# Performance work log

Hardware: AMD Instinct MI355X
Metric: run time of the kernel (lower is better)

## Reference

```python
import jax, jax.numpy as jnp
import numpy as np

POS_THR = 0.7
NEG_THR = 0.3
SAMPLE_BATCH = 256
POS_FRAC = 0.5
B, K, H, W, G = 8, 9, 64, 64, 128
A = K * H * W  # 36864 total anchors


def _make_boxes(key, lead_shape, img=1024.0, wmin=16.0, wmax=256.0):
    k1, k2 = jax.random.split(key)
    ctr = jax.random.uniform(k1, lead_shape + (2,), minval=0.0, maxval=img)
    wh = jax.random.uniform(k2, lead_shape + (2,), minval=wmin, maxval=wmax)
    return jnp.concatenate([ctr - wh / 2, ctr + wh / 2], axis=-1)


def setup_inputs() -> dict:
    key = jax.random.key(0)
    k1, k2, k3, k4 = jax.random.split(key, 4)
    return {
        "cls_logits": jax.random.normal(k1, (B, K, H, W), dtype=jnp.float32),
        "bbox_pred": jax.random.normal(k2, (B, 4 * K, H, W), dtype=jnp.float32) * 0.1,
        "anchors": _make_boxes(k3, (A,)),
        "gt_boxes": _make_boxes(k4, (B, G)),
    }


def _compute_iou(a, g):
    # a: [A,4], g: [G,4] -> [A,G]
    lt = jnp.maximum(a[:, None, :2], g[None, :, :2])
    rb = jnp.minimum(a[:, None, 2:], g[None, :, 2:])
    wh = jnp.clip(rb - lt, 0.0)
    inter = wh[..., 0] * wh[..., 1]
    area_a = (a[:, 2] - a[:, 0]) * (a[:, 3] - a[:, 1])
    area_g = (g[:, 2] - g[:, 0]) * (g[:, 3] - g[:, 1])
    return inter / (area_a[:, None] + area_g[None, :] - inter + 1e-6)


def _encode(anchors, gt):
    aw = anchors[:, 2] - anchors[:, 0]
    ah = anchors[:, 3] - anchors[:, 1]
    acx = (anchors[:, 0] + anchors[:, 2]) / 2
    acy = (anchors[:, 1] + anchors[:, 3]) / 2
    gw = gt[:, 2] - gt[:, 0]
    gh = gt[:, 3] - gt[:, 1]
    gcx = (gt[:, 0] + gt[:, 2]) / 2
    gcy = (gt[:, 1] + gt[:, 3]) / 2
    return jnp.stack([(gcx - acx) / aw, (gcy - acy) / ah,
                      jnp.log(gw / aw), jnp.log(gh / ah)], axis=1)


def _subsample(labels, mask, target, key):
    # deterministic-key analog of torch.randperm subsampling: random priorities,
    # keep the `target` highest-priority anchors of the masked class.
    score = jnp.where(mask, jax.random.uniform(key, labels.shape), -1.0)
    order = jnp.argsort(-score)
    rank = jnp.zeros_like(order).at[order].set(jnp.arange(order.shape[0]))
    keep = mask & (rank < target)
    return jnp.where(mask & ~keep, -1, labels)


def _per_image(cls_i, box_i, anchors, gt, key):
    iou = _compute_iou(anchors, gt)                      # [A,G]
    max_iou = iou.max(axis=1)
    matched_gt_idx = iou.argmax(axis=1)
    labels = jnp.where(max_iou < NEG_THR, 0, -1)
    labels = jnp.where(max_iou >= POS_THR, 1, labels)
    matched_anchor_idx = iou.argmax(axis=0)              # [G]
    labels = labels.at[matched_anchor_idx].set(1)        # force best anchor per gt
    bbox_targets = _encode(anchors, gt[matched_gt_idx])  # [A,4]

    k1, k2 = jax.random.split(key)
    pos_mask0 = labels == 1
    num_pos = pos_mask0.sum()
    target_pos = jnp.minimum(jnp.int32(SAMPLE_BATCH * POS_FRAC), num_pos)
    labels = _subsample(labels, pos_mask0, target_pos, k1)
    neg_mask0 = labels == 0
    num_neg = neg_mask0.sum()
    target_neg = jnp.minimum(SAMPLE_BATCH - target_pos, num_neg)
    labels = _subsample(labels, neg_mask0, target_neg, k2)

    valid = (labels >= 0).astype(cls_i.dtype)
    z = (labels == 1).astype(cls_i.dtype)
    # BCEWithLogits: softplus(x) - x*z
    bce = jax.nn.softplus(cls_i) - cls_i * z
    cls_loss = (bce * valid).sum() / jnp.maximum(valid.sum(), 1.0)

    pos = (labels == 1).astype(cls_i.dtype)
    d = box_i - bbox_targets
    ad = jnp.abs(d)
    sl1 = jnp.where(ad < 1.0, 0.5 * d * d, ad - 0.5)     # SmoothL1, beta=1
    bbox_loss = (sl1 * pos[:, None]).sum() / jnp.maximum(4.0 * pos.sum(), 1.0)
    return cls_loss, bbox_loss


def reference(cls_logits, bbox_pred, anchors, gt_boxes):
    b = cls_logits.shape[0]
    cls = cls_logits.transpose(0, 2, 3, 1).reshape(b, -1)          # [B,A]
    box = bbox_pred.transpose(0, 2, 3, 1).reshape(b, -1, 4)        # [B,A,4]
    keys = jax.random.split(jax.random.key(42), b)
    cls_l, box_l = jax.vmap(_per_image, in_axes=(0, 0, None, 0, 0))(
        cls, box, anchors, gt_boxes, keys)
    cls_loss = cls_l.mean()
    bbox_loss = box_l.mean()
    return jnp.stack([cls_loss, bbox_loss, cls_loss + bbox_loss])
```

## Files before the change

### kernel.cpp

```cpp
#include <hip/hip_runtime.h>
#include <stdint.h>
#include <limits.h>

#define PARTITIONABLE 1

#define B_ 8
#define K_ 9
#define H_ 64
#define W_ 64
#define G_ 128
#define A_ 36864
#define HALF_A 18432
#define QUART_A 9216
#define NBUCK 8192
#define CAP 1024
#define NBEST 4096
#define NLAB  1152

struct KeyParams { uint32_t k[B_][4]; };

__host__ __device__ static inline uint32_t rotl32(uint32_t x, int r) {
  return (x << r) | (x >> (32 - r));
}

__host__ __device__ static inline void tf2x32(uint32_t k0, uint32_t k1,
                                              uint32_t x0, uint32_t x1,
                                              uint32_t& o0, uint32_t& o1) {
  uint32_t ks2 = k0 ^ k1 ^ 0x1BD11BDAu;
  x0 += k0; x1 += k1;
#define TF_R(r) { x0 += x1; x1 = rotl32(x1, r); x1 ^= x0; }
  TF_R(13) TF_R(15) TF_R(26) TF_R(6)
  x0 += k1;  x1 += ks2 + 1u;
  TF_R(17) TF_R(29) TF_R(16) TF_R(24)
  x0 += ks2; x1 += k0 + 2u;
  TF_R(13) TF_R(15) TF_R(26) TF_R(6)
  x0 += k0;  x1 += k1 + 3u;
  TF_R(17) TF_R(29) TF_R(16) TF_R(24)
  x0 += k1;  x1 += ks2 + 4u;
  TF_R(13) TF_R(15) TF_R(26) TF_R(6)
  x0 += ks2; x1 += k0 + 5u;
#undef TF_R
  o0 = x0; o1 = x1;
}

__device__ static inline uint32_t anchor_vbits(uint32_t k0, uint32_t k1, int a) {
  uint32_t o0, o1;
#if PARTITIONABLE
  tf2x32(k0, k1, 0u, (uint32_t)a, o0, o1);
  return (o0 ^ o1) >> 9;
#else
  if (a < HALF_A) { tf2x32(k0, k1, (uint32_t)a, (uint32_t)(a + HALF_A), o0, o1); return o0 >> 9; }
  else            { tf2x32(k0, k1, (uint32_t)(a - HALF_A), (uint32_t)a, o0, o1); return o1 >> 9; }
#endif
}

__device__ static inline float area_of(float x0, float y0, float x1, float y1) {
#pragma clang fp contract(off)
  return (x1 - x0) * (y1 - y0);
}

__device__ static inline float iou_fn(float a0, float a1, float a2, float a3,
                                      float g0, float g1, float g2, float g3) {
#pragma clang fp contract(off)
  float ltx = fmaxf(a0, g0), lty = fmaxf(a1, g1);
  float rbx = fminf(a2, g2), rby = fminf(a3, g3);
  float w = rbx - ltx; w = (w < 0.f) ? 0.f : w;
  float h = rby - lty; h = (h < 0.f) ? 0.f : h;
  float inter  = w * h;
  float area_a = (a2 - a0) * (a3 - a1);
  float area_g = (g2 - g0) * (g3 - g1);
  return inter / (area_a + area_g - inter + 1e-6f);
}

__device__ static inline float iou_pre_a(float a0, float a1, float a2, float a3,
                                         float area_a,
                                         float g0, float g1, float g2, float g3) {
#pragma clang fp contract(off)
  float ltx = fmaxf(a0, g0), lty = fmaxf(a1, g1);
  float rbx = fminf(a2, g2), rby = fminf(a3, g3);
  float w = rbx - ltx; w = (w < 0.f) ? 0.f : w;
  float h = rby - lty; h = (h < 0.f) ? 0.f : h;
  float inter  = w * h;
  float area_g = (g2 - g0) * (g3 - g1);
  return inter / (area_a + area_g - inter + 1e-6f);
}

__device__ static inline void encode4(float4 an, float4 gg, float* tt) {
#pragma clang fp contract(off)
  float aw  = an.z - an.x,            ah  = an.w - an.y;
  float acx = (an.x + an.z) * 0.5f,   acy = (an.y + an.w) * 0.5f;
  float gw  = gg.z - gg.x,            gh  = gg.w - gg.y;
  float gcx = (gg.x + gg.z) * 0.5f,   gcy = (gg.y + gg.w) * 0.5f;
  tt[0] = (gcx - acx) / aw;
  tt[1] = (gcy - acy) / ah;
  tt[2] = logf(gw / aw);
  tt[3] = logf(gh / ah);
}

__device__ static inline int block_reduce_int(int v, int* sh) {
  int t = threadIdx.x;
  sh[t] = v; __syncthreads();
  for (int s = 128; s > 0; s >>= 1) { if (t < s) sh[t] += sh[t + s]; __syncthreads(); }
  int r = sh[0]; __syncthreads();
  return r;
}
__device__ static inline float block_reduce_float(float v, float* sh) {
  int t = threadIdx.x;
  sh[t] = v; __syncthreads();
  for (int s = 128; s > 0; s >>= 1) { if (t < s) sh[t] += sh[t + s]; __syncthreads(); }
  float r = sh[0]; __syncthreads();
  return r;
}

__device__ static inline unsigned long long pack_vi(float v, int a) {
  return ((unsigned long long)__float_as_uint(v) << 32) | (uint32_t)(~(uint32_t)a);
}

__global__ __launch_bounds__(256) void fused_iou_k(const float* __restrict__ anchors,
                                                   const float* __restrict__ gtb,
                                                   int* __restrict__ labels,
                                                   int* __restrict__ mgt,
                                                   uint32_t* __restrict__ vpos,
                                                   uint32_t* __restrict__ vneg,
                                                   int* __restrict__ ghist,
                                                   int* __restrict__ counts,
                                                   unsigned long long* __restrict__ gmax,
                                                   KeyParams kp) {
  __shared__ unsigned long long sp[256];
  __shared__ float4 gts[G_];
  __shared__ int red[256];
  const int bid = blockIdx.x;
  const int t = threadIdx.x;

  if (bid < NBEST) {
    const int bg = bid & 1023;
    const int base = (bid >> 10) * QUART_A;
    float4 gg = ((const float4*)gtb)[bg];
    float v0 = -1.f, v1 = -1.f, v2 = -1.f, v3 = -1.f;
    int   i0 = 0,    i1 = 0,    i2 = 0,    i3 = 0;
    for (int a = base + t; a < base + QUART_A; a += 1024) {
      float4 an0 = ((const float4*)anchors)[a];
      float4 an1 = ((const float4*)anchors)[a + 256];
      float4 an2 = ((const float4*)anchors)[a + 512];
      float4 an3 = ((const float4*)anchors)[a + 768];
      float w0 = iou_fn(an0.x, an0.y, an0.z, an0.w, gg.x, gg.y, gg.z, gg.w);
      float w1 = iou_fn(an1.x, an1.y, an1.z, an1.w, gg.x, gg.y, gg.z, gg.w);
      float w2 = iou_fn(an2.x, an2.y, an2.z, an2.w, gg.x, gg.y, gg.z, gg.w);
      float w3 = iou_fn(an3.x, an3.y, an3.z, an3.w, gg.x, gg.y, gg.z, gg.w);
      if (w0 > v0) { v0 = w0; i0 = a; }
      if (w1 > v1) { v1 = w1; i1 = a + 256; }
      if (w2 > v2) { v2 = w2; i2 = a + 512; }
      if (w3 > v3) { v3 = w3; i3 = a + 768; }
    }
    unsigned long long p = pack_vi(v0, i0);
    unsigned long long q = pack_vi(v1, i1); if (q > p) p = q;
    q = pack_vi(v2, i2); if (q > p) p = q;
    q = pack_vi(v3, i3); if (q > p) p = q;
    sp[t] = p; __syncthreads();
    for (int s = 128; s > 0; s >>= 1) {
      if (t < s) { if (sp[t + s] > sp[t]) sp[t] = sp[t + s]; }
      __syncthreads();
    }
    if (t == 0) atomicMax(&gmax[bg], sp[0]);
    return;
  }

  const int r = bid - NBEST;
  const int b = r / (A_ / 256);
  const int xb = r % (A_ / 256);
  for (int i = t; i < G_; i += 256) gts[i] = ((const float4*)gtb)[b * G_ + i];
  __syncthreads();
  const int a = xb * 256 + t;
  float4 an = ((const float4*)anchors)[a];
  float area_a = area_of(an.x, an.y, an.z, an.w);
  float bv = -1.f; int bi = 0;
#pragma unroll 4
  for (int g = 0; g < G_; g++) {
    float4 gg = gts[g];
    float v = iou_pre_a(an.x, an.y, an.z, an.w, area_a,
                        gg.x, gg.y, gg.z, gg.w);
    if (v > bv) { bv = v; bi = g; }
  }
  int lb = (bv < 0.3f) ? 0 : ((bv >= 0.7f) ? 1 : -1);
  size_t idx = (size_t)b * A_ + a;
  uint32_t vp = anchor_vbits(kp.k[b][0], kp.k[b][1], a);
  uint32_t vn = anchor_vbits(kp.k[b][2], kp.k[b][3], a);
  labels[idx] = lb;
  mgt[idx]    = bi;
  vpos[idx]   = vp;
  vneg[idx]   = vn;
  if (lb == 1)      atomicAdd(&ghist[(b * 2 + 0) * NBUCK + (vp >> 10)], 1);
  else if (lb == 0) atomicAdd(&ghist[(b * 2 + 1) * NBUCK + (vn >> 10)], 1);
  int packed = (lb == 1 ? 1 : 0) | ((lb == 0 ? 1 : 0) << 16);
  int rr = block_reduce_int(packed, red);
  if (t == 0) {
    atomicAdd(&counts[b * 2 + 0], rr & 0xFFFF);
    atomicAdd(&counts[b * 2 + 1], rr >> 16);
  }
}

__global__ void force_k(const unsigned long long* __restrict__ gmax,
                        int* __restrict__ labels,
                        const uint32_t* __restrict__ vpos,
                        const uint32_t* __restrict__ vneg,
                        int* __restrict__ ghist,
                        int* __restrict__ counts) {
  int tg = blockIdx.x * 256 + threadIdx.x;
  int b = tg / G_;
  int a = (int)(~(uint32_t)(gmax[tg] & 0xFFFFFFFFull));
  size_t idx = (size_t)b * A_ + a;
  int old = atomicExch(&labels[idx], 1);
  if (old != 1) {
    atomicAdd(&counts[b * 2 + 0], 1);
    atomicAdd(&ghist[(b * 2 + 0) * NBUCK + (vpos[idx] >> 10)], 1);
    if (old == 0) {
      atomicSub(&counts[b * 2 + 1], 1);
      atomicSub(&ghist[(b * 2 + 1) * NBUCK + (vneg[idx] >> 10)], 1);
    }
  }
}

__global__ __launch_bounds__(256) void cutoff_k(const int* __restrict__ ghist,
                                                const int* __restrict__ counts,
                                                int* __restrict__ cbR,
                                                int* __restrict__ targets) {
  const int row = blockIdx.x;
  const int b = row >> 1, c = row & 1;
  const int t = threadIdx.x;
  __shared__ int seg[256];
  int npos = counts[b * 2 + 0], nneg = counts[b * 2 + 1];
  int tp = npos < 128 ? npos : 128;
  int tn = 256 - tp; if (nneg < tn) tn = nneg;
  const int target = (c == 0) ? tp : tn;
  const int* hist = ghist + (size_t)row * NBUCK;
  { int s = 0; const int base = t * 32;
    for (int i = 0; i < 32; i++) s += hist[base + i];
    seg[t] = s; }
  __syncthreads();
  if (t == 0) {
    int cb = INT_MAX, R = 0;
    if (target > 0) {
      int cum = 0, si = -1;
      for (int i = 255; i >= 0; i--) { if (cum + seg[i] >= target) { si = i; break; } cum += seg[i]; }
      for (int j = si * 32 + 31; j >= si * 32; j--) {
        if (cum + hist[j] >= target) { cb = j; R = target - cum; break; }
        cum += hist[j];
      }
    }
    cbR[row * 2 + 0] = cb;
    cbR[row * 2 + 1] = R;
    targets[row] = target;
  }
}

__global__ __launch_bounds__(256) void cand_k(const int* __restrict__ labels,
                                              const uint32_t* __restrict__ vpos,
                                              const uint32_t* __restrict__ vneg,
                                              const int* __restrict__ cbR,
                                              int* __restrict__ ccnt,
                                              uint32_t* __restrict__ cvv,
                                              int* __restrict__ cii) {
  const int b = blockIdx.y;
  const int a = blockIdx.x * 256 + threadIdx.x;
  size_t idx = (size_t)b * A_ + a;
  int lb = labels[idx];
  if (lb < 0) return;
  int c = (lb == 1) ? 0 : 1;
  int row = b * 2 + c;
  uint32_t v = (c == 0 ? vpos : vneg)[idx];
  if ((int)(v >> 10) == cbR[row * 2]) {
    int p = atomicAdd(&ccnt[row], 1);
    if (p < CAP) { cvv[row * CAP + p] = v; cii[row * CAP + p] = a; }
  }
}

__global__ __launch_bounds__(256) void loss_k(const float* __restrict__ anchors,
                                              const float* __restrict__ gtb,
                                              const float* __restrict__ cls,
                                              const float* __restrict__ boxp,
                                              const int* __restrict__ labels,
                                              const int* __restrict__ mgt,
                                              const uint32_t* __restrict__ vpos,
                                              const uint32_t* __restrict__ vneg,
                                              const int* __restrict__ cbR,
                                              const int* __restrict__ ccnt,
                                              const uint32_t* __restrict__ cvv,
                                              const int* __restrict__ cii,
                                              float* __restrict__ bsums) {
  const int b = blockIdx.y;
  const int a = blockIdx.x * 256 + threadIdx.x;
  const int t = threadIdx.x;
  __shared__ float redf[256];
  float sb = 0.f, ss = 0.f;
  size_t idx = (size_t)b * A_ + a;
  int lb = labels[idx];
  if (lb >= 0) {
    int c = (lb == 1) ? 0 : 1;
    int row = b * 2 + c;
    uint32_t v = (c == 0 ? vpos : vneg)[idx];
    int bucket = (int)(v >> 10);
    int cb = cbR[row * 2];
    bool kept = bucket > cb;
    if (!kept && bucket == cb) {
      int c2 = ccnt[row]; if (c2 > CAP) c2 = CAP;
      int R = cbR[row * 2 + 1];
      int r = 0;
      for (int j = 0; j < c2; j++) {
        uint32_t vj = cvv[row * CAP + j]; int ij = cii[row * CAP + j];
        if (vj > v || (vj == v && ij < a)) r++;
      }
      kept = (r < R);
    }
    if (kept) {
      int kk = a % K_; int hw = a / K_; int hh = hw / W_; int wx = hw % W_;
      float x  = cls[(((size_t)b * K_ + kk) * H_ + hh) * W_ + wx];
      float sp = fmaxf(x, 0.f) + log1pf(expf(-fabsf(x)));
      sb = (lb == 1) ? (sp - x) : sp;
      if (lb == 1) {
        float4 an = ((const float4*)anchors)[a];
        int    mg = mgt[idx];
        float4 gg = ((const float4*)gtb)[b * G_ + mg];
        float tt[4]; encode4(an, gg, tt);
        for (int cc = 0; cc < 4; cc++) {
          float p = boxp[(((size_t)b * (4 * K_) + (4 * kk + cc)) * H_ + hh) * W_ + wx];
          float d = p - tt[cc];
          float ad = fabsf(d);
          ss += (ad < 1.f) ? (0.5f * d * d) : (ad - 0.5f);
        }
      }
    }
  }
  float sbT = block_reduce_float(sb, redf);
  float ssT = block_reduce_float(ss, redf);
  if (t == 0) {
    if (sbT != 0.f) atomicAdd(&bsums[b * 2 + 0], sbT);
    if (ssT != 0.f) atomicAdd(&bsums[b * 2 + 1], ssT);
  }
}

__global__ void final_k(const float* __restrict__ bsums, const int* __restrict__ targets,
                        float* __restrict__ out) {
  if (threadIdx.x == 0 && blockIdx.x == 0) {
    float cl = 0.f, bl = 0.f;
    for (int b = 0; b < B_; b++) {
      int tp = targets[b * 2 + 0], tn = targets[b * 2 + 1];
      cl += bsums[b * 2 + 0] / fmaxf((float)(tp + tn), 1.f);
      bl += bsums[b * 2 + 1] / fmaxf(4.f * (float)tp, 1.f);
    }
    cl *= 0.125f; bl *= 0.125f;
    out[0] = cl; out[1] = bl; out[2] = cl + bl;
  }
}

static void compute_keys(KeyParams& kp) {
  const uint32_t r0 = 0u, r1 = 42u;
#if PARTITIONABLE
  for (int b = 0; b < B_; b++) {
    uint32_t kb0, kb1;
    tf2x32(r0, r1, 0u, (uint32_t)b, kb0, kb1);
    uint32_t a0, a1, c0, c1;
    tf2x32(kb0, kb1, 0u, 0u, a0, a1);
    tf2x32(kb0, kb1, 0u, 1u, c0, c1);
    kp.k[b][0] = a0; kp.k[b][1] = a1; kp.k[b][2] = c0; kp.k[b][3] = c1;
  }
#else
  uint32_t o0[8], o1[8], flat[16];
  for (int i = 0; i < 8; i++) tf2x32(r0, r1, (uint32_t)i, (uint32_t)(8 + i), o0[i], o1[i]);
  for (int i = 0; i < 8; i++) { flat[i] = o0[i]; flat[8 + i] = o1[i]; }
  for (int b = 0; b < B_; b++) {
    uint32_t kb0 = flat[2 * b], kb1 = flat[2 * b + 1];
    uint32_t a0, b0, a1, b1;
    tf2x32(kb0, kb1, 0u, 2u, a0, b0);
    tf2x32(kb0, kb1, 1u, 3u, a1, b1);
    kp.k[b][0] = a0; kp.k[b][1] = a1; kp.k[b][2] = b0; kp.k[b][3] = b1;
  }
#endif
}

extern "C" void kernel_launch(void* const* d_in, const int* in_sizes, int n_in,
                              void* d_out, int out_size, void* d_ws, size_t ws_size,
                              hipStream_t stream) {
  const float* cls     = (const float*)d_in[0];
  const float* boxp    = (const float*)d_in[1];
  const float* anchors = (const float*)d_in[2];
  const float* gtb     = (const float*)d_in[3];
  float* out = (float*)d_out;

  uint8_t* w = (uint8_t*)d_ws;
  unsigned long long* gmax = (unsigned long long*)w;
  int*      ghist   = (int*)(w + 8192);
  int*      counts  = (int*)(w + 532480);
  int*      ccnt    = counts + 16;
  float*    bsums   = (float*)(ccnt + 16);
  int*      labels  = (int*)(w + 532672);
  int*      mgt     = labels + (size_t)B_ * A_;
  uint32_t* vpos    = (uint32_t*)(mgt + (size_t)B_ * A_);
  uint32_t* vneg    = vpos + (size_t)B_ * A_;
  int*      cbR     = (int*)(vneg + (size_t)B_ * A_);
  int*      targets = cbR + 32;
  uint32_t* cvv     = (uint32_t*)(targets + 16);
  int*      cii     = (int*)(cvv + 16 * CAP);

  KeyParams kp;
  compute_keys(kp);

  (void)hipMemsetAsync(w, 0, 532672, stream);
  fused_iou_k<<<NBEST + NLAB, 256, 0, stream>>>(anchors, gtb, labels, mgt,
                                                vpos, vneg, ghist, counts, gmax, kp);
  force_k<<<(B_ * G_) / 256, 256, 0, stream>>>(gmax, labels, vpos, vneg, ghist, counts);
  cutoff_k<<<16, 256, 0, stream>>>(ghist, counts, cbR, targets);
  cand_k<<<dim3(A_ / 256, B_), 256, 0, stream>>>(labels, vpos, vneg, cbR, ccnt, cvv, cii);
  loss_k<<<dim3(A_ / 256, B_), 256, 0, stream>>>(anchors, gtb, cls, boxp, labels, mgt,
                                                 vpos, vneg, cbR, ccnt, cvv, cii, bsums);
  final_k<<<1, 64, 0, stream>>>(bsums, targets, out);
}
```

Baseline: 175.7 us.

## Fuse per-GT best-anchor search into per-anchor IoU pass via LDS atomics

Removes the separate 4096 blocks that recomputed IoU per GT box to find each GT's best anchor. The per-anchor label blocks now also produce it: each thread visits the GT boxes in a staggered order (starting at its own lane modulo 128) and does shared-memory 64-bit atomicMax into duplicated per-GT slots. The slots are then merged and pushed to global gmax. This halves the IoU computation but adds one LDS atomic per IoU, which may contend or serialize. Argmax tie-breaking is preserved through packed value and index encoding.

```diff
diff --git a/kernel.cpp b/kernel.cpp
--- a/kernel.cpp
+++ b/kernel.cpp
@@ -11,10 +11,8 @@
 #define G_ 128
 #define A_ 36864
 #define HALF_A 18432
-#define QUART_A 9216
 #define NBUCK 8192
 #define CAP 1024
-#define NBEST 4096
 #define NLAB  1152
 
 struct KeyParams { uint32_t k[B_][4]; };
@@ -59,19 +57,6 @@
   return (x1 - x0) * (y1 - y0);
 }
 
-__device__ static inline float iou_fn(float a0, float a1, float a2, float a3,
-                                      float g0, float g1, float g2, float g3) {
-#pragma clang fp contract(off)
-  float ltx = fmaxf(a0, g0), lty = fmaxf(a1, g1);
-  float rbx = fminf(a2, g2), rby = fminf(a3, g3);
-  float w = rbx - ltx; w = (w < 0.f) ? 0.f : w;
-  float h = rby - lty; h = (h < 0.f) ? 0.f : h;
-  float inter  = w * h;
-  float area_a = (a2 - a0) * (a3 - a1);
-  float area_g = (g2 - g0) * (g3 - g1);
-  return inter / (area_a + area_g - inter + 1e-6f);
-}
-
 __device__ static inline float iou_pre_a(float a0, float a1, float a2, float a3,
                                          float area_a,
                                          float g0, float g1, float g2, float g3) {
@@ -112,10 +97,6 @@
   return r;
 }
 
-__device__ static inline unsigned long long pack_vi(float v, int a) {
-  return ((unsigned long long)__float_as_uint(v) << 32) | (uint32_t)(~(uint32_t)a);
-}
-
 __global__ __launch_bounds__(256) void fused_iou_k(const float* __restrict__ anchors,
                                                    const float* __restrict__ gtb,
                                                    int* __restrict__ labels,
@@ -126,61 +107,53 @@
                                                    int* __restrict__ counts,
                                                    unsigned long long* __restrict__ gmax,
                                                    KeyParams kp) {
-  __shared__ unsigned long long sp[256];
-  __shared__ float4 gts[G_];
+  __shared__ float2 gp01[2 * G_];
+  __shared__ float2 gp23[2 * G_];
+  __shared__ unsigned long long slot2[2 * G_];
   __shared__ int red[256];
   const int bid = blockIdx.x;
   const int t = threadIdx.x;
-
-  if (bid < NBEST) {
-    const int bg = bid & 1023;
-    const int base = (bid >> 10) * QUART_A;
-    float4 gg = ((const float4*)gtb)[bg];
-    float v0 = -1.f, v1 = -1.f, v2 = -1.f, v3 = -1.f;
-    int   i0 = 0,    i1 = 0,    i2 = 0,    i3 = 0;
-    for (int a = base + t; a < base + QUART_A; a += 1024) {
-      float4 an0 = ((const float4*)anchors)[a];
-      float4 an1 = ((const float4*)anchors)[a + 256];
-      float4 an2 = ((const float4*)anchors)[a + 512];
-      float4 an3 = ((const float4*)anchors)[a + 768];
-      float w0 = iou_fn(an0.x, an0.y, an0.z, an0.w, gg.x, gg.y, gg.z, gg.w);
-      float w1 = iou_fn(an1.x, an1.y, an1.z, an1.w, gg.x, gg.y, gg.z, gg.w);
-      float w2 = iou_fn(an2.x, an2.y, an2.z, an2.w, gg.x, gg.y, gg.z, gg.w);
-      float w3 = iou_fn(an3.x, an3.y, an3.z, an3.w, gg.x, gg.y, gg.z, gg.w);
-      if (w0 > v0) { v0 = w0; i0 = a; }
-      if (w1 > v1) { v1 = w1; i1 = a + 256; }
-      if (w2 > v2) { v2 = w2; i2 = a + 512; }
-      if (w3 > v3) { v3 = w3; i3 = a + 768; }
-    }
-    unsigned long long p = pack_vi(v0, i0);
-    unsigned long long q = pack_vi(v1, i1); if (q > p) p = q;
-    q = pack_vi(v2, i2); if (q > p) p = q;
-    q = pack_vi(v3, i3); if (q > p) p = q;
-    sp[t] = p; __syncthreads();
-    for (int s = 128; s > 0; s >>= 1) {
-      if (t < s) { if (sp[t + s] > sp[t]) sp[t] = sp[t + s]; }
-      __syncthreads();
-    }
-    if (t == 0) atomicMax(&gmax[bg], sp[0]);
-    return;
-  }
-
-  const int r = bid - NBEST;
-  const int b = r / (A_ / 256);
-  const int xb = r % (A_ / 256);
-  for (int i = t; i < G_; i += 256) gts[i] = ((const float4*)gtb)[b * G_ + i];
+  const int b  = bid / (A_ / 256);
+  const int xb = bid % (A_ / 256);
+
+  if (t < G_) {
+    float4 gg = ((const float4*)gtb)[b * G_ + t];
+    float2 p01; p01.x = gg.x; p01.y = gg.y;
+    float2 p23; p23.x = gg.z; p23.y = gg.w;
+    gp01[t] = p01; gp01[t + G_] = p01;
+    gp23[t] = p23; gp23[t + G_] = p23;
+  }
+  slot2[t] = 0ull;
   __syncthreads();
+
   const int a = xb * 256 + t;
   float4 an = ((const float4*)anchors)[a];
   float area_a = area_of(an.x, an.y, an.z, an.w);
-  float bv = -1.f; int bi = 0;
+  const int t7 = t & (G_ - 1);
+  const unsigned long long alow = (unsigned long long)(~(uint32_t)a);
+  unsigned long long blp = 0ull;
 #pragma unroll 4
-  for (int g = 0; g < G_; g++) {
-    float4 gg = gts[g];
+  for (int s = 0; s < G_; s++) {
+    const int gi = t7 + s;
+    float2 p01 = gp01[gi];
+    float2 p23 = gp23[gi];
     float v = iou_pre_a(an.x, an.y, an.z, an.w, area_a,
-                        gg.x, gg.y, gg.z, gg.w);
-    if (v > bv) { bv = v; bi = g; }
-  }
+                        p01.x, p01.y, p23.x, p23.y);
+    unsigned long long hi = (unsigned long long)__float_as_uint(v) << 32;
+    unsigned long long lp = hi | (unsigned)((gi & (G_ - 1)) ^ (G_ - 1));
+    if (lp > blp) blp = lp;
+    atomicMax(&slot2[gi], hi | alow);
+  }
+  __syncthreads();
+  if (t < G_) {
+    unsigned long long p = slot2[t];
+    unsigned long long q = slot2[t + G_];
+    if (q > p) p = q;
+    atomicMax(&gmax[b * G_ + t], p);
+  }
+
+  float bv = __uint_as_float((uint32_t)(blp >> 32));
+  int   bi = ((int)(blp & (unsigned long long)(G_ - 1))) ^ (G_ - 1);
   int lb = (bv < 0.3f) ? 0 : ((bv >= 0.7f) ? 1 : -1);
   size_t idx = (size_t)b * A_ + a;
   uint32_t vp = anchor_vbits(kp.k[b][0], kp.k[b][1], a);
@@ -405,8 +378,8 @@
   compute_keys(kp);
 
   (void)hipMemsetAsync(w, 0, 532672, stream);
-  fused_iou_k<<<NBEST + NLAB, 256, 0, stream>>>(anchors, gtb, labels, mgt,
-                                                vpos, vneg, ghist, counts, gmax, kp);
+  fused_iou_k<<<NLAB, 256, 0, stream>>>(anchors, gtb, labels, mgt,
+                                        vpos, vneg, ghist, counts, gmax, kp);
   force_k<<<(B_ * G_) / 256, 256, 0, stream>>>(gmax, labels, vpos, vneg, ghist, counts);
   cutoff_k<<<16, 256, 0, stream>>>(ghist, counts, cbR, targets);
   cand_k<<<dim3(A_ / 256, B_), 256, 0, stream>>>(labels, vpos, vneg, cbR, ccnt, cvv, cii);
```

Result: faster. 150.5 us (-14.3%).
